# Optimization experiments

Measured on AMD Instinct MI355X. Metric: run time of the kernel, lower is better.

## Reference

```python
import jax, jax.numpy as jnp
import numpy as np

B = 4096
N = 8192
LEVEL_SIZES = [8, 128, 2048, 6008]  # sums to N; 4-level taxonomy
EPS = 1e-07


def _build_hierarchy():
    """parent[c] = parent node index (-1 for roots); level_of[c] = depth."""
    rng = np.random.default_rng(0)
    parent = np.full(N, -1, np.int32)
    level_of = np.zeros(N, np.int32)
    off, prev_start, prev_size = 0, 0, 0
    for l, sz in enumerate(LEVEL_SIZES):
        level_of[off:off + sz] = l
        if l > 0:
            parent[off:off + sz] = rng.integers(prev_start, prev_start + prev_size, sz)
        prev_start, prev_size = off, sz
        off += sz
    return parent, level_of


def setup_inputs() -> dict:
    key = jax.random.key(0)
    k1, k2 = jax.random.split(key)
    pred = jax.random.normal(k1, (B, N), dtype=jnp.float32)  # logits
    target = (jax.random.uniform(k2, (B, N)) < 0.02).astype(jnp.float32)
    parent_np, level_np = _build_hierarchy()
    return {
        "pred": pred,
        "target": target,
        "parent": jnp.asarray(parent_np),
        "level_of": jnp.asarray(level_np),
        "mode": 0,  # 0 = EVAL (propagate conditional probs), 1 = TRAIN
    }


def reference(pred, target, parent, level_of, mode):
    p = jax.nn.sigmoid(pred)                      # [B, N]
    parent_clip = jnp.maximum(parent, 0)          # safe gather index for roots
    is_root = parent < 0                          # recursive_relation[-1]

    if mode != 1:  # not 'TRAIN': top-down conditional probability propagation
        pc = p
        for l in range(1, len(LEVEL_SIZES)):
            # pred_clone[:, children(n)] = pred[:, children] * pred_clone[:, n]
            pc = jnp.where(level_of == l, p * pc[:, parent_clip], pc)
        pred_clone = pc
    else:
        pred_clone = None

    # mask[b, c] = 1 if c is a root, or if target[b, parent[c]] == 1
    mask = jnp.where(is_root, jnp.float32(1.0), target[:, parent_clip])

    pcl = jnp.clip(p, EPS, 1.0 - EPS)
    loss = -(jnp.log(pcl) * target + (1.0 - target) * mask * jnp.log(1.0 - pcl))
    loss = loss.sum(axis=1).mean()
    return (loss, pred_clone)
```

## Files before the change

kernel.cpp:

```cpp
#include <hip/hip_runtime.h>


#define N_NODES 8192
#define L1S 8
#define L2S 136
#define L3S 2184
#define EPSF 1e-7f

__device__ __forceinline__ float sigmoidf(float x) {
    return 1.0f / (1.0f + __expf(-x));
}

__global__ __launch_bounds__(256) void cs_main(
    const float* __restrict__ pred,
    const float* __restrict__ target,
    const int* __restrict__ parent,
    float* __restrict__ out,
    float* __restrict__ bsum,
    float inv_b)
{
    __shared__ float pc[L3S];
    __shared__ float tg[L3S];
    __shared__ float red[4];

    const int tid = threadIdx.x;
    const int b = blockIdx.x;
    const float* __restrict__ prow = pred + (size_t)b * N_NODES;
    const float* __restrict__ trow = target + (size_t)b * N_NODES;
    float* __restrict__ orow = out + 1 + (size_t)b * N_NODES;

    float lsum = 0.0f;

    for (int c4 = tid; c4 < L3S / 4; c4 += 256) {
        const int c0 = c4 * 4;
        const float4 x4 = ((const float4*)prow)[c4];
        const float4 t4 = ((const float4*)trow)[c4];
        const int4  q4 = ((const int4*)parent)[c4];
        const float xs[4] = {x4.x, x4.y, x4.z, x4.w};
        const float ts[4] = {t4.x, t4.y, t4.z, t4.w};
        const int   qs[4] = {q4.x, q4.y, q4.z, q4.w};
#pragma unroll
        for (int j = 0; j < 4; ++j) {
            const float p = sigmoidf(xs[j]);
            pc[c0 + j] = p;
            tg[c0 + j] = ts[j];
            const float mask = (qs[j] < 0) ? 1.0f : trow[qs[j]];
            const float pcl = fminf(fmaxf(p, EPSF), 1.0f - EPSF);
            lsum -= __logf(pcl) * ts[j] + (1.0f - ts[j]) * mask * __logf(1.0f - pcl);
        }
    }
    __syncthreads();
    for (int c = L1S + tid; c < L2S; c += 256) pc[c] *= pc[parent[c]];
    __syncthreads();
    for (int c = L2S + tid; c < L3S; c += 256) pc[c] *= pc[parent[c]];
    __syncthreads();
    for (int c = tid; c < L3S; c += 256) orow[c] = pc[c];

    for (int c4 = L3S / 4 + tid; c4 < N_NODES / 4; c4 += 256) {
        const int c0 = c4 * 4;
        const float4 x4 = ((const float4*)prow)[c4];
        const float4 t4 = ((const float4*)trow)[c4];
        const int4  q4 = ((const int4*)parent)[c4];
        const float xs[4] = {x4.x, x4.y, x4.z, x4.w};
        const float ts[4] = {t4.x, t4.y, t4.z, t4.w};
        const int   qs[4] = {q4.x, q4.y, q4.z, q4.w};
#pragma unroll
        for (int j = 0; j < 4; ++j) {
            const float p = sigmoidf(xs[j]);
            const int pa = qs[j];
            const float mask = tg[pa];
            const float pcl = fminf(fmaxf(p, EPSF), 1.0f - EPSF);
            lsum -= __logf(pcl) * ts[j] + (1.0f - ts[j]) * mask * __logf(1.0f - pcl);
            orow[c0 + j] = p * pc[pa];
        }
    }

#pragma unroll
    for (int off = 32; off > 0; off >>= 1) lsum += __shfl_down(lsum, off);
    if ((tid & 63) == 0) red[tid >> 6] = lsum;
    __syncthreads();
    if (tid == 0) {
        const float s = (red[0] + red[1]) + (red[2] + red[3]);
        if (bsum) bsum[blockIdx.x] = s;
        else atomicAdd(out, s * inv_b);
    }
}

__global__ __launch_bounds__(256) void cs_finish(
    const float* __restrict__ bsum, float* __restrict__ out,
    int nblocks, float inv_b)
{
    __shared__ float red[4];
    const int tid = threadIdx.x;
    float s = 0.0f;
    for (int i = tid; i < nblocks; i += 256) s += bsum[i];
#pragma unroll
    for (int off = 32; off > 0; off >>= 1) s += __shfl_down(s, off);
    if ((tid & 63) == 0) red[tid >> 6] = s;
    __syncthreads();
    if (tid == 0) out[0] = ((red[0] + red[1]) + (red[2] + red[3])) * inv_b;
}

extern "C" void kernel_launch(void* const* d_in, const int* in_sizes, int n_in,
                              void* d_out, int out_size, void* d_ws, size_t ws_size,
                              hipStream_t stream) {
    const float* pred   = (const float*)d_in[0];
    const float* target = (const float*)d_in[1];
    const int*   parent = (const int*)d_in[2];

    float* out = (float*)d_out;
    const int batch = in_sizes[0] / N_NODES;
    const float inv_b = 1.0f / (float)batch;

    if (ws_size >= (size_t)batch * sizeof(float)) {
        float* bsum = (float*)d_ws;
        cs_main<<<batch, 256, 0, stream>>>(pred, target, parent, out, bsum, inv_b);
        cs_finish<<<1, 256, 0, stream>>>(bsum, out, batch, inv_b);
    } else {
        hipMemsetAsync(d_out, 0, sizeof(float), stream);
        cs_main<<<batch, 256, 0, stream>>>(pred, target, parent, out, nullptr, inv_b);
    }
}
```

Before: 91.07 us.

## Use softplus loss form, interleave shared arrays, fuse level output, prefetch tail

```diff
diff --git a/kernel.cpp b/kernel.cpp
--- a/kernel.cpp
+++ b/kernel.cpp
@@ -5,11 +5,10 @@
 #define L1S 8
 #define L2S 136
 #define L3S 2184
-#define EPSF 1e-7f
+#define N4   (N_NODES / 4)
+#define L3S4 (L3S / 4)
 
-__device__ __forceinline__ float sigmoidf(float x) {
-    return 1.0f / (1.0f + __expf(-x));
-}
+__device__ __forceinline__ float frcp(float x) { return __builtin_amdgcn_rcpf(x); }
 
 __global__ __launch_bounds__(256) void cs_main(
     const float* __restrict__ pred,
@@ -19,8 +18,7 @@
     float* __restrict__ bsum,
     float inv_b)
 {
-    __shared__ float pc[L3S];
-    __shared__ float tg[L3S];
+    __shared__ float2 pt[L3S];
     __shared__ float red[4];
 
     const int tid = threadIdx.x;
@@ -31,7 +29,7 @@
 
     float lsum = 0.0f;
 
-    for (int c4 = tid; c4 < L3S / 4; c4 += 256) {
+    for (int c4 = tid; c4 < L3S4; c4 += 256) {
         const int c0 = c4 * 4;
         const float4 x4 = ((const float4*)prow)[c4];
         const float4 t4 = ((const float4*)trow)[c4];
@@ -41,38 +39,61 @@
         const int   qs[4] = {q4.x, q4.y, q4.z, q4.w};
 #pragma unroll
         for (int j = 0; j < 4; ++j) {
-            const float p = sigmoidf(xs[j]);
-            pc[c0 + j] = p;
-            tg[c0 + j] = ts[j];
+            const float x = xs[j], t = ts[j];
+            const float e = __expf(-x);
+            const float p = frcp(1.0f + e);
+            const float s = __logf(1.0f + e);
             const float mask = (qs[j] < 0) ? 1.0f : trow[qs[j]];
-            const float pcl = fminf(fmaxf(p, EPSF), 1.0f - EPSF);
-            lsum -= __logf(pcl) * ts[j] + (1.0f - ts[j]) * mask * __logf(1.0f - pcl);
+            lsum += t * s + (1.0f - t) * mask * (s + x);
+            pt[c0 + j] = make_float2(p, t);
         }
     }
     __syncthreads();
-    for (int c = L1S + tid; c < L2S; c += 256) pc[c] *= pc[parent[c]];
+
+    for (int c = L1S + tid; c < L2S; c += 256) pt[c].x *= pt[parent[c]].x;
     __syncthreads();
-    for (int c = L2S + tid; c < L3S; c += 256) pc[c] *= pc[parent[c]];
+
+    for (int c = tid; c < L3S; c += 256) {
+        if (c < L2S) {
+            orow[c] = pt[c].x;
+        } else {
+            const float v = pt[c].x * pt[parent[c]].x;
+            pt[c].x = v;
+            orow[c] = v;
+        }
+    }
     __syncthreads();
-    for (int c = tid; c < L3S; c += 256) orow[c] = pc[c];
 
-    for (int c4 = L3S / 4 + tid; c4 < N_NODES / 4; c4 += 256) {
+    int c4 = L3S4 + tid;
+    float4 x4, t4; int4 q4;
+    if (c4 < N4) {
+        x4 = ((const float4*)prow)[c4];
+        t4 = ((const float4*)trow)[c4];
+        q4 = ((const int4*)parent)[c4];
+    }
+    while (c4 < N4) {
+        const int n4 = c4 + 256;
+        float4 nx, nt; int4 nq;
+        if (n4 < N4) {
+            nx = ((const float4*)prow)[n4];
+            nt = ((const float4*)trow)[n4];
+            nq = ((const int4*)parent)[n4];
+        }
         const int c0 = c4 * 4;
-        const float4 x4 = ((const float4*)prow)[c4];
-        const float4 t4 = ((const float4*)trow)[c4];
-        const int4  q4 = ((const int4*)parent)[c4];
         const float xs[4] = {x4.x, x4.y, x4.z, x4.w};
         const float ts[4] = {t4.x, t4.y, t4.z, t4.w};
         const int   qs[4] = {q4.x, q4.y, q4.z, q4.w};
 #pragma unroll
         for (int j = 0; j < 4; ++j) {
-            const float p = sigmoidf(xs[j]);
-            const int pa = qs[j];
-            const float mask = tg[pa];
-            const float pcl = fminf(fmaxf(p, EPSF), 1.0f - EPSF);
-            lsum -= __logf(pcl) * ts[j] + (1.0f - ts[j]) * mask * __logf(1.0f - pcl);
-            orow[c0 + j] = p * pc[pa];
+            const float x = xs[j], t = ts[j];
+            const float2 pm = pt[qs[j]];
+            const float e = __expf(-x);
+            const float p = frcp(1.0f + e);
+            const float s = __logf(1.0f + e);
+            lsum += t * s + (1.0f - t) * pm.y * (s + x);
+            orow[c0 + j] = p * pm.x;
         }
+        x4 = nx; t4 = nt; q4 = nq; c4 = n4;
     }
 
 #pragma unroll
```

Result: slower. 92.94 us (+2.1%).

## Process one row per wavefront with sign-packed target and software-pipelined loads

Applied to the files above, without the earlier changes.

```diff
diff --git a/kernel.cpp b/kernel.cpp
--- a/kernel.cpp
+++ b/kernel.cpp
@@ -1,99 +1,162 @@
 #include <hip/hip_runtime.h>
 
+
+typedef float f4 __attribute__((ext_vector_type(4)));
+typedef float f2 __attribute__((ext_vector_type(2)));
+typedef int   i4 __attribute__((ext_vector_type(4)));
 
 #define N_NODES 8192
 #define L1S 8
 #define L2S 136
 #define L3S 2184
-#define EPSF 1e-7f
+#define N4   2048
+#define L3S4 546
+#define WPB 4
 
-__device__ __forceinline__ float sigmoidf(float x) {
-    return 1.0f / (1.0f + __expf(-x));
+__device__ __forceinline__ float frcp(float x) { return __builtin_amdgcn_rcpf(x); }
+
+__device__ __forceinline__ void wave_sync() {
+    __builtin_amdgcn_sched_barrier(0);
+    asm volatile("s_waitcnt lgkmcnt(0)" ::: "memory");
+    __builtin_amdgcn_wave_barrier();
+    __builtin_amdgcn_sched_barrier(0);
 }
 
-__global__ __launch_bounds__(256) void cs_main(
+__global__ __launch_bounds__(256, 4) void cs_main(
     const float* __restrict__ pred,
     const float* __restrict__ target,
     const int* __restrict__ parent,
     float* __restrict__ out,
     float* __restrict__ bsum,
-    float inv_b)
+    float inv_b, int nrows)
 {
-    __shared__ float pc[L3S];
-    __shared__ float tg[L3S];
-    __shared__ float red[4];
+    __shared__ float pk_all[WPB * L3S];
 
     const int tid = threadIdx.x;
-    const int b = blockIdx.x;
+    const int lane = tid & 63;
+    const int wid = tid >> 6;
+    const int b = blockIdx.x * WPB + wid;
+    if (b >= nrows) return;
+
+    float* __restrict__ mypk = pk_all + wid * L3S;
     const float* __restrict__ prow = pred + (size_t)b * N_NODES;
     const float* __restrict__ trow = target + (size_t)b * N_NODES;
     float* __restrict__ orow = out + 1 + (size_t)b * N_NODES;
+    const f4* __restrict__ Pp = (const f4*)prow;
+    const f4* __restrict__ Tp = (const f4*)trow;
+    const i4* __restrict__ Qp = (const i4*)parent;
 
     float lsum = 0.0f;
 
-    for (int c4 = tid; c4 < L3S / 4; c4 += 256) {
-        const int c0 = c4 * 4;
-        const float4 x4 = ((const float4*)prow)[c4];
-        const float4 t4 = ((const float4*)trow)[c4];
-        const int4  q4 = ((const int4*)parent)[c4];
-        const float xs[4] = {x4.x, x4.y, x4.z, x4.w};
-        const float ts[4] = {t4.x, t4.y, t4.z, t4.w};
-        const int   qs[4] = {q4.x, q4.y, q4.z, q4.w};
+    {
+        int g = lane;
+        f4 x4 = Pp[g], t4 = Tp[g];
 #pragma unroll
-        for (int j = 0; j < 4; ++j) {
-            const float p = sigmoidf(xs[j]);
-            pc[c0 + j] = p;
-            tg[c0 + j] = ts[j];
-            const float mask = (qs[j] < 0) ? 1.0f : trow[qs[j]];
-            const float pcl = fminf(fmaxf(p, EPSF), 1.0f - EPSF);
-            lsum -= __logf(pcl) * ts[j] + (1.0f - ts[j]) * mask * __logf(1.0f - pcl);
+        for (int k = 0; k < 9; ++k) {
+            const int gn = g + 64;
+            f4 nx, nt;
+            const bool hn = (gn < L3S4);
+            if (hn) { nx = Pp[gn]; nt = Tp[gn]; }
+            if (g < L3S4) {
+                f4 pkv;
+#pragma unroll
+                for (int j = 0; j < 4; ++j) {
+                    const float p = frcp(1.0f + __expf(-x4[j]));
+                    pkv[j] = t4[j] > 0.5f ? -p : p;
+                }
+                *(f4*)(mypk + 4 * g) = pkv;
+            }
+            x4 = nx; t4 = nt; g = gn;
         }
     }
-    __syncthreads();
-    for (int c = L1S + tid; c < L2S; c += 256) pc[c] *= pc[parent[c]];
-    __syncthreads();
-    for (int c = L2S + tid; c < L3S; c += 256) pc[c] *= pc[parent[c]];
-    __syncthreads();
-    for (int c = tid; c < L3S; c += 256) orow[c] = pc[c];
 
-    for (int c4 = L3S / 4 + tid; c4 < N_NODES / 4; c4 += 256) {
-        const int c0 = c4 * 4;
-        const float4 x4 = ((const float4*)prow)[c4];
-        const float4 t4 = ((const float4*)trow)[c4];
-        const int4  q4 = ((const int4*)parent)[c4];
-        const float xs[4] = {x4.x, x4.y, x4.z, x4.w};
-        const float ts[4] = {t4.x, t4.y, t4.z, t4.w};
-        const int   qs[4] = {q4.x, q4.y, q4.z, q4.w};
+    int gc = L3S4 + lane;
+    f4 xA = Pp[gc], tA = Tp[gc]; i4 qA = Qp[gc];
+    const int g1 = gc + 64;
+    f4 xB = Pp[g1], tB = Tp[g1]; i4 qB = Qp[g1];
+
+    wave_sync();
+
+    if (lane < L1S) {
+        const float v = mypk[lane];
+        const float p = fabsf(v);
+        lsum += (v < 0.0f) ? -__logf(p) : -__logf(1.0f - p);
+        orow[lane] = p;
+    }
+
 #pragma unroll
-        for (int j = 0; j < 4; ++j) {
-            const float p = sigmoidf(xs[j]);
-            const int pa = qs[j];
-            const float mask = tg[pa];
-            const float pcl = fminf(fmaxf(p, EPSF), 1.0f - EPSF);
-            lsum -= __logf(pcl) * ts[j] + (1.0f - ts[j]) * mask * __logf(1.0f - pcl);
-            orow[c0 + j] = p * pc[pa];
+    for (int k = 0; k < 2; ++k) {
+        const int c = L1S + lane + 64 * k;
+        const int pa = parent[c];
+        const float v = mypk[c];
+        const float pv = mypk[pa];
+        const float p = fabsf(v);
+        const float cum = p * fabsf(pv);
+        const float mask = (pv < 0.0f) ? 1.0f : 0.0f;
+        lsum += (v < 0.0f) ? -__logf(p) : mask * (-__logf(1.0f - p));
+        orow[c] = cum;
+        mypk[c] = (v < 0.0f) ? -cum : cum;
+    }
+    wave_sync();
+
+#pragma unroll 4
+    for (int k = 0; k < 32; ++k) {
+        const int c = L2S + lane + 64 * k;
+        const int pa = parent[c];
+        const float v = mypk[c];
+        const float pv = mypk[pa];
+        const float p = fabsf(v);
+        const float cum = p * fabsf(pv);
+        const float mask = (pv < 0.0f) ? 1.0f : 0.0f;
+        lsum += (v < 0.0f) ? -__logf(p) : mask * (-__logf(1.0f - p));
+        orow[c] = cum;
+        mypk[c] = (v < 0.0f) ? -cum : cum;
+    }
+    wave_sync();
+
+#pragma unroll 4
+    for (int k = 0; k < 24; ++k) {
+        const int gn = gc + 128 > N4 - 1 ? N4 - 1 : gc + 128;
+        f4 nx = Pp[gn], nt = Tp[gn]; i4 nq = Qp[gn];
+        if (gc < N4) {
+            float rr[4];
+#pragma unroll
+            for (int j = 0; j < 4; ++j) {
+                const float x = xA[j], t = tA[j];
+                const float pv = mypk[qA[j]];
+                const float mask = (pv < 0.0f) ? 1.0f : 0.0f;
+                const float e = __expf(-x);
+                const float s = __logf(1.0f + e);
+                const float p = frcp(1.0f + e);
+                lsum += t * s + (1.0f - t) * mask * (s + x);
+                rr[j] = p * fabsf(pv);
+            }
+            float* slot = orow + 4 * gc;
+            slot[0] = rr[0];
+            *(f2*)(slot + 1) = f2{rr[1], rr[2]};
+            slot[3] = rr[3];
         }
+        xA = xB; tA = tB; qA = qB;
+        xB = nx; tB = nt; qB = nq;
+        gc += 64;
     }
 
 #pragma unroll
     for (int off = 32; off > 0; off >>= 1) lsum += __shfl_down(lsum, off);
-    if ((tid & 63) == 0) red[tid >> 6] = lsum;
-    __syncthreads();
-    if (tid == 0) {
-        const float s = (red[0] + red[1]) + (red[2] + red[3]);
-        if (bsum) bsum[blockIdx.x] = s;
-        else atomicAdd(out, s * inv_b);
+    if (lane == 0) {
+        if (bsum) bsum[b] = lsum;
+        else atomicAdd(out, lsum * inv_b);
     }
 }
 
 __global__ __launch_bounds__(256) void cs_finish(
     const float* __restrict__ bsum, float* __restrict__ out,
-    int nblocks, float inv_b)
+    int n, float inv_b)
 {
     __shared__ float red[4];
     const int tid = threadIdx.x;
     float s = 0.0f;
-    for (int i = tid; i < nblocks; i += 256) s += bsum[i];
+    for (int i = tid; i < n; i += 256) s += bsum[i];
 #pragma unroll
     for (int off = 32; off > 0; off >>= 1) s += __shfl_down(s, off);
     if ((tid & 63) == 0) red[tid >> 6] = s;
@@ -111,13 +174,14 @@
     float* out = (float*)d_out;
     const int batch = in_sizes[0] / N_NODES;
     const float inv_b = 1.0f / (float)batch;
+    const int nblk = (batch + WPB - 1) / WPB;
 
     if (ws_size >= (size_t)batch * sizeof(float)) {
         float* bsum = (float*)d_ws;
-        cs_main<<<batch, 256, 0, stream>>>(pred, target, parent, out, bsum, inv_b);
+        cs_main<<<nblk, 256, 0, stream>>>(pred, target, parent, out, bsum, inv_b, batch);
         cs_finish<<<1, 256, 0, stream>>>(bsum, out, batch, inv_b);
     } else {
         hipMemsetAsync(d_out, 0, sizeof(float), stream);
-        cs_main<<<batch, 256, 0, stream>>>(pred, target, parent, out, nullptr, inv_b);
+        cs_main<<<nblk, 256, 0, stream>>>(pred, target, parent, out, nullptr, inv_b, batch);
     }
 }
```

Result: slower. 99.47 us (+9.2%).
